# Kernel tuning notes

Hardware: AMD Instinct MI355X
Metric: run time of the kernel (lower is better)

The kernel has to match this reference:

```python
import jax, jax.numpy as jnp
import numpy as np

N_NEIGHBORS = 5


def setup_inputs() -> dict:
    key = jax.random.key(0)
    k1, k2, k3 = jax.random.split(key, 3)
    B, N, D = 2048, 100000, 128
    x = jax.random.normal(k1, (B, D), dtype=jnp.float32)
    train_data = jax.random.normal(k2, (N, D), dtype=jnp.float32)
    train_labels = jax.random.normal(k3, (N,), dtype=jnp.float32)
    return {"x": x, "train_data": train_data, "train_labels": train_labels}


def reference(x, train_data, train_labels):
    # Euclidean (minkowski p=2) pairwise distances [B, N] via the GEMM
    x2 = jnp.sum(x * x, axis=1, keepdims=True)            # [B,1]
    t2 = jnp.sum(train_data * train_data, axis=1)          # [N]
    d2 = x2 - 2.0 * (x @ train_data.T) + t2[None, :]       # [B,N]
    dist = jnp.sqrt(jnp.maximum(d2, 0.0))

    # k smallest distances (torch.topk largest=False)
    neg_d, idx = jax.lax.top_k(-dist, N_NEIGHBORS)         # [B,k]
    d = -neg_d

    labels = train_labels[idx]                             # [B,k]

    # weights = 'distance': inverse distance, with exact-match handling
    d_inv = 1.0 / d
    inf_mask = jnp.isinf(d_inv)
    inf_row = jnp.any(inf_mask, axis=1, keepdims=True)
    w = jnp.where(inf_row, inf_mask.astype(jnp.float32), d_inv)  # [B,k]

    out = jnp.sum(w * labels, axis=1) / jnp.sum(w, axis=1)  # [B]
    return out
```

## Files before the change

### kernel.cpp

```cpp
#include <hip/hip_runtime.h>
#include <math.h>

typedef __attribute__((ext_vector_type(8))) short bf16x8;
typedef __attribute__((ext_vector_type(4))) float f32x4;
typedef unsigned short ushortT;
typedef unsigned int uint32;

#define KNN_K   5
#define DIM     128
#define FLT_BIG 3.402823466e38f
#define KEY_C   512.0f

#define MF_B     2048
#define MF_N     100000
#define MF_QPB   256
#define MF_QPW   64
#define MF_NCH   250
#define MF_CHS   400
#define MF_TILES (MF_CHS / 16)
#define MF_CSLOT 4
#define MF_NCAND (MF_NCH * MF_CSLOT)
#define MF_RESCORE 10

__device__ __forceinline__ uint32 umn(uint32 a, uint32 b) { return a < b ? a : b; }
__device__ __forceinline__ uint32 umx(uint32 a, uint32 b) { return a > b ? a : b; }

#define TOP5_INSERT(v, id)                                                  \
    if ((v) < bd4) {                                                        \
        bool l0 = (v) < bd0, l1 = (v) < bd1, l2 = (v) < bd2, l3 = (v) < bd3;\
        if (l3) { bd4 = bd3; bi4 = bi3; } else { bd4 = (v); bi4 = (id); }   \
        if (l2) { bd3 = bd2; bi3 = bi2; } else if (l3) { bd3 = (v); bi3 = (id); } \
        if (l1) { bd2 = bd1; bi2 = bi1; } else if (l2) { bd2 = (v); bi2 = (id); } \
        if (l0) { bd1 = bd0; bi1 = bi0; } else if (l1) { bd1 = (v); bi1 = (id); } \
        if (l0) { bd0 = (v); bi0 = (id); }                                  \
    }

__device__ __forceinline__ uint32 f2bf_u(float f) {
    unsigned u = __float_as_uint(f);
    u += 0x7fffu + ((u >> 16) & 1u);
    return u >> 16;
}

__global__ __launch_bounds__(256) void prep_kernel(const float* __restrict__ in,
                                                   ushortT* __restrict__ outbf,
                                                   float* __restrict__ t2c, int rows) {
    const int wv = threadIdx.x >> 6, lane = threadIdx.x & 63;
    const int row = (blockIdx.x * 4 + wv) * 16 + (lane >> 2);
    if (row >= rows) return;
    const int seg = (lane & 3) * 32;
    const float4* p = (const float4*)(in + (size_t)row * DIM + seg);

    float4 v[8];
#pragma unroll
    for (int j = 0; j < 8; ++j) v[j] = p[j];

    uint32 u[16];
#pragma unroll
    for (int j = 0; j < 8; ++j) {
        u[2 * j]     = f2bf_u(v[j].x) | (f2bf_u(v[j].y) << 16);
        u[2 * j + 1] = f2bf_u(v[j].z) | (f2bf_u(v[j].w) << 16);
    }
    uint4* o = (uint4*)(outbf + (size_t)row * DIM + seg);
#pragma unroll
    for (int j = 0; j < 4; ++j)
        o[j] = make_uint4(u[4 * j], u[4 * j + 1], u[4 * j + 2], u[4 * j + 3]);

    float s = 0.f;
#pragma unroll
    for (int j = 0; j < 8; ++j)
        s += v[j].x * v[j].x + v[j].y * v[j].y + v[j].z * v[j].z + v[j].w * v[j].w;
    s += __shfl_xor(s, 1);
    s += __shfl_xor(s, 2);
    if ((lane & 3) == 0) t2c[row] = -(s + KEY_C) * 0.5f;
}

__global__ __launch_bounds__(256) void knn_mfma(
        const ushortT* __restrict__ xbf, const ushortT* __restrict__ tbf,
        const float* __restrict__ t2c,
        uint32* __restrict__ cand_k, uint32* __restrict__ cand_i) {
    __shared__ uint32 sk[4][MF_QPW][12];

    const int tid  = threadIdx.x;
    const int wv   = tid >> 6;
    const int lane = tid & 63;
    const int quad = lane >> 4;
    const int c16  = lane & 15;
    const int chunk = blockIdx.x;
    const int qbase = blockIdx.y * MF_QPB + wv * MF_QPW;
    const int n0 = chunk * MF_CHS;

    bf16x8 bq[4][4];
#pragma unroll
    for (int t = 0; t < 4; ++t)
#pragma unroll
        for (int s = 0; s < 4; ++s)
            bq[t][s] = *(const bf16x8*)(xbf + (size_t)(qbase + t * 16 + c16) * DIM
                                        + s * 32 + quad * 8);

    uint32 L[4][3];
#pragma unroll
    for (int t = 0; t < 4; ++t) { L[t][0] = 0xFFFFFFFFu; L[t][1] = 0xFFFFFFFFu; L[t][2] = 0xFFFFFFFFu; }

    const ushortT* ap = tbf + (size_t)(n0 + c16) * DIM + quad * 8;
    const float*   tp = t2c + n0 + quad * 4;

    bf16x8 fa[4];
#pragma unroll
    for (int s = 0; s < 4; ++s) fa[s] = *(const bf16x8*)(ap + s * 32);
    float4 tv = *(const float4*)tp;

    int locb = quad * 4;
    for (int tile = 0; tile < MF_TILES; ++tile) {
        const int nx = (tile + 1 < MF_TILES) ? tile + 1 : 0;
        const ushortT* np = ap + (size_t)nx * (16 * DIM);
        bf16x8 fb[4];
#pragma unroll
        for (int s = 0; s < 4; ++s) fb[s] = *(const bf16x8*)(np + s * 32);
        float4 tn = *(const float4*)(tp + nx * 16);

        f32x4 acc[4];
#pragma unroll
        for (int t = 0; t < 4; ++t) acc[t] = (f32x4){tv.x, tv.y, tv.z, tv.w};
#pragma unroll
        for (int s = 0; s < 4; ++s)
#pragma unroll
            for (int t = 0; t < 4; ++t)
                acc[t] = __builtin_amdgcn_mfma_f32_16x16x32_bf16(
                             fa[s], bq[t][s], acc[t], 0, 0, 0);

#pragma unroll
        for (int t = 0; t < 4; ++t) {
            uint32 p0 = (__float_as_uint(acc[t][0]) & 0xFFFFFC00u) | (uint32)(locb + 0);
            uint32 p1 = (__float_as_uint(acc[t][1]) & 0xFFFFFC00u) | (uint32)(locb + 1);
            uint32 p2 = (__float_as_uint(acc[t][2]) & 0xFFFFFC00u) | (uint32)(locb + 2);
            uint32 p3 = (__float_as_uint(acc[t][3]) & 0xFFFFFC00u) | (uint32)(locb + 3);
            uint32 m0 = umn(p0, p1), M0 = umx(p0, p1);
            uint32 m1 = umn(p2, p3), M1 = umx(p2, p3);
            uint32 s0 = umn(m0, m1);
            uint32 c  = umx(m0, m1), d = umn(M0, M1);
            uint32 s1 = umn(c, d),   s2 = umx(c, d);
            uint32 a0 = L[t][0], a1 = L[t][1], a2 = L[t][2];
            uint32 cc = umx(a0, s0), dd = umn(a1, s1);
            uint32 ee = umx(a1, s1), ff = umn(a2, s2);
            L[t][0] = umn(a0, s0);
            L[t][1] = umn(cc, dd);
            L[t][2] = umn(umx(cc, dd), umn(ee, ff));
        }
        locb += 16;
#pragma unroll
        for (int s = 0; s < 4; ++s) fa[s] = fb[s];
        tv = tn;
    }

#pragma unroll
    for (int t = 0; t < 4; ++t)
#pragma unroll
        for (int j = 0; j < 3; ++j)
            sk[wv][t * 16 + c16][quad * 3 + j] = L[t][j];
    __syncthreads();

    const int mw = tid >> 6, ml = tid & 63;
    uint32 k0 = 0xFFFFFFFFu, k1 = 0xFFFFFFFFu, k2 = 0xFFFFFFFFu, k3 = 0xFFFFFFFFu;
#pragma unroll
    for (int j = 0; j < 12; ++j) {
        uint32 v = sk[mw][ml][j];
        uint32 t0 = umx(k0, v);
        k0 = umn(k0, v);
        uint32 t1 = umx(k1, t0);
        k1 = umn(k1, t0);
        uint32 t2_ = umx(k2, t1);
        k2 = umn(k2, t1);
        k3 = umn(k3, t2_);
    }
    const size_t base = ((size_t)(blockIdx.y * MF_QPB + tid) * MF_NCH + chunk)
                        * MF_CSLOT;
    uint4 kk; kk.x = k0; kk.y = k1; kk.z = k2; kk.w = k3;
    uint4 ii; ii.x = n0 + (k0 & 1023u); ii.y = n0 + (k1 & 1023u);
    ii.z = n0 + (k2 & 1023u); ii.w = n0 + (k3 & 1023u);
    *(uint4*)(cand_k + base) = kk;
    *(uint4*)(cand_i + base) = ii;
}

__global__ __launch_bounds__(64) void knn_final(
        const uint32* __restrict__ cand_k, const uint32* __restrict__ cand_i,
        const float* __restrict__ x, const float* __restrict__ train,
        const float* __restrict__ labels, float* __restrict__ out) {
    const int q = blockIdx.x;
    const int lane = threadIdx.x;
    const float xa = x[(size_t)q * DIM + lane];
    const float xb = x[(size_t)q * DIM + 64 + lane];

    uint32 ck[16]; uint32 cid[16];
    const size_t cb = (size_t)q * MF_NCAND;
#pragma unroll
    for (int j = 0; j < 16; ++j) {
        int p = lane + 64 * j;
        if (p < MF_NCAND) { ck[j] = cand_k[cb + p]; cid[j] = cand_i[cb + p]; }
        else { ck[j] = 0xFFFFFFFFu; cid[j] = 0x7FFFFFFFu; }
    }

    uint32 selid[MF_RESCORE];
    uint32 tk = 0, ti = 0; bool first = true;
#pragma unroll
    for (int round = 0; round < MF_RESCORE; ++round) {
        uint32 mk = 0xFFFFFFFFu, mi = 0xFFFFFFFFu;
#pragma unroll
        for (int j = 0; j < 16; ++j) {
            bool gt = first || (ck[j] > tk) || (ck[j] == tk && cid[j] > ti);
            if (gt && ((ck[j] < mk) || (ck[j] == mk && cid[j] < mi))) {
                mk = ck[j]; mi = cid[j];
            }
        }
#pragma unroll
        for (int off = 32; off; off >>= 1) {
            uint32 ok = __shfl_xor(mk, off);
            uint32 oi = __shfl_xor(mi, off);
            if (ok < mk || (ok == mk && oi < mi)) { mk = ok; mi = oi; }
        }
        selid[round] = mi;
        tk = mk; ti = mi; first = false;
    }

    float d2v[MF_RESCORE];
#pragma unroll
    for (int r = 0; r < MF_RESCORE; ++r) {
        const float* tr = train + (size_t)selid[r] * DIM;
        float da = xa - tr[lane];
        float db = xb - tr[64 + lane];
        d2v[r] = fmaf(da, da, db * db);
    }
#pragma unroll
    for (int r = 0; r < MF_RESCORE; ++r) {
#pragma unroll
        for (int off = 32; off; off >>= 1) d2v[r] += __shfl_xor(d2v[r], off);
    }

    float bd0 = FLT_BIG, bd1 = FLT_BIG, bd2 = FLT_BIG, bd3 = FLT_BIG, bd4 = FLT_BIG;
    int   bi0 = 0, bi1 = 0, bi2 = 0, bi3 = 0, bi4 = 0;
#pragma unroll
    for (int r = 0; r < MF_RESCORE; ++r) {
        float v = d2v[r]; int id = (int)selid[r];
        TOP5_INSERT(v, id);
    }

    float d0 = sqrtf(fmaxf(bd0, 0.f));
    float d1 = sqrtf(fmaxf(bd1, 0.f));
    float d2_ = sqrtf(fmaxf(bd2, 0.f));
    float d3 = sqrtf(fmaxf(bd3, 0.f));
    float d4 = sqrtf(fmaxf(bd4, 0.f));
    bool zero = (d0 == 0.f) || (d1 == 0.f) || (d2_ == 0.f) || (d3 == 0.f) || (d4 == 0.f);
    float w0, w1, w2, w3, w4;
    if (zero) {
        w0 = (d0 == 0.f) ? 1.f : 0.f;
        w1 = (d1 == 0.f) ? 1.f : 0.f;
        w2 = (d2_ == 0.f) ? 1.f : 0.f;
        w3 = (d3 == 0.f) ? 1.f : 0.f;
        w4 = (d4 == 0.f) ? 1.f : 0.f;
    } else {
        w0 = 1.f / d0; w1 = 1.f / d1; w2 = 1.f / d2_; w3 = 1.f / d3; w4 = 1.f / d4;
    }
    float wsum = w0 + w1 + w2 + w3 + w4;
    float lsum = w0 * labels[bi0] + w1 * labels[bi1] + w2 * labels[bi2]
               + w3 * labels[bi3] + w4 * labels[bi4];
    if (lane == 0) out[q] = lsum / wsum;
}

#define FB_QT     16
#define FB_NCHUNK 25
#define FB_NT     256

__global__ void rowsq_kernel(const float* __restrict__ data,
                             float* __restrict__ out, int rows) {
    int r = blockIdx.x * blockDim.x + threadIdx.x;
    if (r >= rows) return;
    const float4* p = (const float4*)(data + (size_t)r * DIM);
    float s0 = 0.f, s1 = 0.f, s2 = 0.f, s3 = 0.f;
#pragma unroll
    for (int i = 0; i < DIM / 4; ++i) {
        float4 v = p[i];
        s0 += v.x * v.x; s1 += v.y * v.y; s2 += v.z * v.z; s3 += v.w * v.w;
    }
    out[r] = (s0 + s1) + (s2 + s3);
}

__global__ __launch_bounds__(FB_NT) void fb_phaseA(
        const float* __restrict__ x, const float* __restrict__ train,
        const float* __restrict__ x2, const float* __restrict__ t2,
        float* __restrict__ cand_d, int* __restrict__ cand_i,
        int N, int chunkSize) {
    __shared__ float xs[FB_QT][DIM + 4];
    __shared__ float rd[FB_QT][16 * KNN_K];
    __shared__ int   ri[FB_QT][16 * KNN_K];

    const int q0 = blockIdx.x * FB_QT;
    const int chunk = blockIdx.y;
    const int n0 = chunk * chunkSize;
    const int n1 = min(n0 + chunkSize, N);
    const int t = threadIdx.x;

    for (int i = t; i < FB_QT * DIM; i += FB_NT) {
        int q = i >> 7, d = i & (DIM - 1);
        xs[q][d] = x[(size_t)(q0 + q) * DIM + d];
    }
    __syncthreads();

    const int q  = t & (FB_QT - 1);
    const int ln = t >> 4;
    const float myx2 = x2[q0 + q];
    const float4* xp = (const float4*)xs[q];

    float bd0 = FLT_BIG, bd1 = FLT_BIG, bd2 = FLT_BIG, bd3 = FLT_BIG, bd4 = FLT_BIG;
    int   bi0 = -1, bi1 = -1, bi2 = -1, bi3 = -1, bi4 = -1;

    int n = n0 + ln;
    for (; n < n1; n += 16) {
        const float4* r0 = (const float4*)(train + (size_t)n * DIM);
        float dA = 0.f;
#pragma unroll 8
        for (int i = 0; i < DIM / 4; ++i) {
            float4 a = xp[i], b0 = r0[i];
            dA += a.x * b0.x + a.y * b0.y + a.z * b0.z + a.w * b0.w;
        }
        float vA = myx2 - 2.f * dA + t2[n];
        TOP5_INSERT(vA, n);
    }

    rd[q][ln * KNN_K + 0] = bd0;  ri[q][ln * KNN_K + 0] = bi0;
    rd[q][ln * KNN_K + 1] = bd1;  ri[q][ln * KNN_K + 1] = bi1;
    rd[q][ln * KNN_K + 2] = bd2;  ri[q][ln * KNN_K + 2] = bi2;
    rd[q][ln * KNN_K + 3] = bd3;  ri[q][ln * KNN_K + 3] = bi3;
    rd[q][ln * KNN_K + 4] = bd4;  ri[q][ln * KNN_K + 4] = bi4;
    __syncthreads();

    if (t < FB_QT) {
        float* dq = rd[t]; int* iq = ri[t];
        size_t base = ((size_t)(q0 + t) * FB_NCHUNK + chunk) * KNN_K;
#pragma unroll
        for (int k = 0; k < KNN_K; ++k) {
            float best = FLT_BIG; int bj = 0;
            for (int j = 0; j < 16 * KNN_K; ++j) {
                float v = dq[j];
                if (v < best) { best = v; bj = j; }
            }
            cand_d[base + k] = best; cand_i[base + k] = iq[bj];
            dq[bj] = FLT_BIG;
        }
    }
}

__global__ void fb_phaseB(const float* __restrict__ cand_d,
                          const int* __restrict__ cand_i,
                          const float* __restrict__ labels,
                          float* __restrict__ out, int B, int ncand) {
    int qq = blockIdx.x * blockDim.x + threadIdx.x;
    if (qq >= B) return;
    const float* cd = cand_d + (size_t)qq * ncand;
    const int*   ci = cand_i + (size_t)qq * ncand;

    float bd0 = FLT_BIG, bd1 = FLT_BIG, bd2 = FLT_BIG, bd3 = FLT_BIG, bd4 = FLT_BIG;
    int   bi0 = -1, bi1 = -1, bi2 = -1, bi3 = -1, bi4 = -1;
    for (int j = 0; j < ncand; ++j) {
        float v = cd[j]; int id = ci[j];
        TOP5_INSERT(v, id);
    }
    float d0 = sqrtf(fmaxf(bd0, 0.f));
    float d1 = sqrtf(fmaxf(bd1, 0.f));
    float d2 = sqrtf(fmaxf(bd2, 0.f));
    float d3 = sqrtf(fmaxf(bd3, 0.f));
    float d4 = sqrtf(fmaxf(bd4, 0.f));
    bool zero = (d0 == 0.f) || (d1 == 0.f) || (d2 == 0.f) || (d3 == 0.f) || (d4 == 0.f);
    float w0, w1, w2, w3, w4;
    if (zero) {
        w0 = (d0 == 0.f) ? 1.f : 0.f;
        w1 = (d1 == 0.f) ? 1.f : 0.f;
        w2 = (d2 == 0.f) ? 1.f : 0.f;
        w3 = (d3 == 0.f) ? 1.f : 0.f;
        w4 = (d4 == 0.f) ? 1.f : 0.f;
    } else {
        w0 = 1.f / d0; w1 = 1.f / d1; w2 = 1.f / d2; w3 = 1.f / d3; w4 = 1.f / d4;
    }
    float wsum = w0 + w1 + w2 + w3 + w4;
    float lsum = w0 * labels[bi0] + w1 * labels[bi1] + w2 * labels[bi2]
               + w3 * labels[bi3] + w4 * labels[bi4];
    out[qq] = lsum / wsum;
}

static inline size_t align256(size_t v) { return (v + 255) & ~(size_t)255; }

extern "C" void kernel_launch(void* const* d_in, const int* in_sizes, int n_in,
                              void* d_out, int out_size, void* d_ws, size_t ws_size,
                              hipStream_t stream) {
    const float* x      = (const float*)d_in[0];
    const float* train  = (const float*)d_in[1];
    const float* labels = (const float*)d_in[2];

    const int N = in_sizes[2];
    const int D = in_sizes[1] / N;
    const int B = in_sizes[0] / D;
    (void)n_in;

    size_t o_tbf = 0;
    size_t o_xbf = align256(o_tbf + (size_t)N * DIM * sizeof(ushortT));
    size_t o_t2c = align256(o_xbf + (size_t)B * DIM * sizeof(ushortT));
    size_t o_x2d = align256(o_t2c + (size_t)N * sizeof(float));
    size_t o_ck  = align256(o_x2d + (size_t)B * sizeof(float));
    size_t o_ci  = align256(o_ck + (size_t)B * MF_NCAND * sizeof(uint32));
    size_t need  = align256(o_ci + (size_t)B * MF_NCAND * sizeof(uint32));

    const bool mfma_ok = (N == MF_N) && (D == DIM) && (B == MF_B) && (ws_size >= need);

    if (mfma_ok) {
        ushortT* tbf = (ushortT*)((char*)d_ws + o_tbf);
        ushortT* xbf = (ushortT*)((char*)d_ws + o_xbf);
        float* t2c   = (float*)((char*)d_ws + o_t2c);
        float* x2d   = (float*)((char*)d_ws + o_x2d);
        uint32* cand_k = (uint32*)((char*)d_ws + o_ck);
        uint32* cand_i = (uint32*)((char*)d_ws + o_ci);

        prep_kernel<<<(N + 63) / 64, 256, 0, stream>>>(train, tbf, t2c, N);
        prep_kernel<<<(B + 63) / 64, 256, 0, stream>>>(x, xbf, x2d, B);

        dim3 gridA(MF_NCH, MF_B / MF_QPB);
        knn_mfma<<<gridA, 256, 0, stream>>>(xbf, tbf, t2c, cand_k, cand_i);
        knn_final<<<MF_B, 64, 0, stream>>>(cand_k, cand_i, x, train, labels,
                                           (float*)d_out);
    } else {
        float* t2     = (float*)d_ws;
        float* x2v    = t2 + N;
        float* cand_d = x2v + B;
        int*   cand_i = (int*)(cand_d + (size_t)B * FB_NCHUNK * KNN_K);

        rowsq_kernel<<<(N + 255) / 256, 256, 0, stream>>>(train, t2, N);
        rowsq_kernel<<<(B + 255) / 256, 256, 0, stream>>>(x, x2v, B);
        const int chunkSize = (N + FB_NCHUNK - 1) / FB_NCHUNK;
        dim3 gridA(B / FB_QT, FB_NCHUNK);
        fb_phaseA<<<gridA, FB_NT, 0, stream>>>(x, train, x2v, t2,
                                               cand_d, cand_i, N, chunkSize);
        fb_phaseB<<<(B + 255) / 256, 256, 0, stream>>>(cand_d, cand_i, labels,
                                                       (float*)d_out, B,
                                                       FB_NCHUNK * KNN_K);
    }
}
```

Baseline: 237.1 us.

## Pad train chunks to 256, swizzle block mapping, drop candidate index buffer

Pads the training set to 256 chunks, with padding rows given a sentinel norm term, so the candidate count per query divides evenly into the final-kernel lanes. The 2D grid becomes a 1D launch whose block ids are swizzled so groups of 8 chunks are processed across all 8 query groups together, aiming for better L2 reuse of train tiles. Candidate indices are no longer written to memory; the final kernel rebuilds them from slot position and the low key bits, halving candidate traffic. The tile loop is manually double-buffered in pairs. The cost is a few extra padded chunks of work, and the padding keys must never be selected.

```diff
diff --git a/kernel.cpp b/kernel.cpp
--- a/kernel.cpp
+++ b/kernel.cpp
@@ -15,9 +15,10 @@
 #define MF_N     100000
 #define MF_QPB   256
 #define MF_QPW   64
-#define MF_NCH   250
+#define MF_NCH   256
 #define MF_CHS   400
-#define MF_TILES (MF_CHS / 16)
+#define MF_NPAD  (MF_NCH * MF_CHS)
+#define MF_TILES 25
 #define MF_CSLOT 4
 #define MF_NCAND (MF_NCH * MF_CSLOT)
 #define MF_RESCORE 10
@@ -43,10 +44,15 @@
 
 __global__ __launch_bounds__(256) void prep_kernel(const float* __restrict__ in,
                                                    ushortT* __restrict__ outbf,
-                                                   float* __restrict__ t2c, int rows) {
+                                                   float* __restrict__ t2c,
+                                                   int rowsValid, int rowsTotal) {
     const int wv = threadIdx.x >> 6, lane = threadIdx.x & 63;
     const int row = (blockIdx.x * 4 + wv) * 16 + (lane >> 2);
-    if (row >= rows) return;
+    if (row >= rowsTotal) return;
+    if (row >= rowsValid) {
+        if ((lane & 3) == 0) t2c[row] = -1e30f;
+        return;
+    }
     const int seg = (lane & 3) * 32;
     const float4* p = (const float4*)(in + (size_t)row * DIM + seg);
 
@@ -76,17 +82,19 @@
 
 __global__ __launch_bounds__(256) void knn_mfma(
         const ushortT* __restrict__ xbf, const ushortT* __restrict__ tbf,
-        const float* __restrict__ t2c,
-        uint32* __restrict__ cand_k, uint32* __restrict__ cand_i) {
+        const float* __restrict__ t2c, uint32* __restrict__ cand_k) {
     __shared__ uint32 sk[4][MF_QPW][12];
 
+    const int id   = blockIdx.x;
+    const int r8   = id & 7, g = id >> 3;
+    const int chunk = ((g >> 3) << 3) | r8;
+    const int jq   = g & 7;
     const int tid  = threadIdx.x;
     const int wv   = tid >> 6;
     const int lane = tid & 63;
     const int quad = lane >> 4;
     const int c16  = lane & 15;
-    const int chunk = blockIdx.x;
-    const int qbase = blockIdx.y * MF_QPB + wv * MF_QPW;
+    const int qbase = jq * MF_QPB + wv * MF_QPW;
     const int n0 = chunk * MF_CHS;
 
     bf16x8 bq[4][4];
@@ -104,20 +112,7 @@
     const ushortT* ap = tbf + (size_t)(n0 + c16) * DIM + quad * 8;
     const float*   tp = t2c + n0 + quad * 4;
 
-    bf16x8 fa[4];
-#pragma unroll
-    for (int s = 0; s < 4; ++s) fa[s] = *(const bf16x8*)(ap + s * 32);
-    float4 tv = *(const float4*)tp;
-
-    int locb = quad * 4;
-    for (int tile = 0; tile < MF_TILES; ++tile) {
-        const int nx = (tile + 1 < MF_TILES) ? tile + 1 : 0;
-        const ushortT* np = ap + (size_t)nx * (16 * DIM);
-        bf16x8 fb[4];
-#pragma unroll
-        for (int s = 0; s < 4; ++s) fb[s] = *(const bf16x8*)(np + s * 32);
-        float4 tn = *(const float4*)(tp + nx * 16);
-
+    auto process = [&](bf16x8 (&F)[4], float4 tv, int locb) {
         f32x4 acc[4];
 #pragma unroll
         for (int t = 0; t < 4; ++t) acc[t] = (f32x4){tv.x, tv.y, tv.z, tv.w};
@@ -126,8 +121,7 @@
 #pragma unroll
             for (int t = 0; t < 4; ++t)
                 acc[t] = __builtin_amdgcn_mfma_f32_16x16x32_bf16(
-                             fa[s], bq[t][s], acc[t], 0, 0, 0);
-
+                             F[s], bq[t][s], acc[t], 0, 0, 0);
 #pragma unroll
         for (int t = 0; t < 4; ++t) {
             uint32 p0 = (__float_as_uint(acc[t][0]) & 0xFFFFFC00u) | (uint32)(locb + 0);
@@ -146,11 +140,27 @@
             L[t][1] = umn(cc, dd);
             L[t][2] = umn(umx(cc, dd), umn(ee, ff));
         }
-        locb += 16;
-#pragma unroll
-        for (int s = 0; s < 4; ++s) fa[s] = fb[s];
-        tv = tn;
-    }
+    };
+
+    bf16x8 fa[4], fb[4];
+    float4 tva, tvb;
+#pragma unroll
+    for (int s = 0; s < 4; ++s) fa[s] = *(const bf16x8*)(ap + s * 32);
+    tva = *(const float4*)tp;
+
+    int locb = quad * 4;
+    for (int it = 0; it < 12; ++it) {
+#pragma unroll
+        for (int s = 0; s < 4; ++s) fb[s] = *(const bf16x8*)(ap + 16 * DIM + s * 32);
+        tvb = *(const float4*)(tp + 16);
+        process(fa, tva, locb);
+#pragma unroll
+        for (int s = 0; s < 4; ++s) fa[s] = *(const bf16x8*)(ap + 32 * DIM + s * 32);
+        tva = *(const float4*)(tp + 32);
+        process(fb, tvb, locb + 16);
+        ap += 32 * DIM; tp += 32; locb += 32;
+    }
+    process(fa, tva, locb);
 
 #pragma unroll
     for (int t = 0; t < 4; ++t)
@@ -172,17 +182,13 @@
         k2 = umn(k2, t1);
         k3 = umn(k3, t2_);
     }
-    const size_t base = ((size_t)(blockIdx.y * MF_QPB + tid) * MF_NCH + chunk)
-                        * MF_CSLOT;
+    const size_t base = ((size_t)(jq * MF_QPB + tid) * MF_NCH + chunk) * MF_CSLOT;
     uint4 kk; kk.x = k0; kk.y = k1; kk.z = k2; kk.w = k3;
-    uint4 ii; ii.x = n0 + (k0 & 1023u); ii.y = n0 + (k1 & 1023u);
-    ii.z = n0 + (k2 & 1023u); ii.w = n0 + (k3 & 1023u);
     *(uint4*)(cand_k + base) = kk;
-    *(uint4*)(cand_i + base) = ii;
 }
 
 __global__ __launch_bounds__(64) void knn_final(
-        const uint32* __restrict__ cand_k, const uint32* __restrict__ cand_i,
+        const uint32* __restrict__ cand_k,
         const float* __restrict__ x, const float* __restrict__ train,
         const float* __restrict__ labels, float* __restrict__ out) {
     const int q = blockIdx.x;
@@ -194,9 +200,10 @@
     const size_t cb = (size_t)q * MF_NCAND;
 #pragma unroll
     for (int j = 0; j < 16; ++j) {
-        int p = lane + 64 * j;
-        if (p < MF_NCAND) { ck[j] = cand_k[cb + p]; cid[j] = cand_i[cb + p]; }
-        else { ck[j] = 0xFFFFFFFFu; cid[j] = 0x7FFFFFFFu; }
+        const int p = lane + 64 * j;
+        uint32 k = cand_k[cb + p];
+        ck[j] = k;
+        cid[j] = (uint32)(p >> 2) * MF_CHS + (k & 1023u);
     }
 
     uint32 selid[MF_RESCORE];
@@ -400,12 +407,10 @@
     (void)n_in;
 
     size_t o_tbf = 0;
-    size_t o_xbf = align256(o_tbf + (size_t)N * DIM * sizeof(ushortT));
+    size_t o_xbf = align256(o_tbf + (size_t)MF_NPAD * DIM * sizeof(ushortT));
     size_t o_t2c = align256(o_xbf + (size_t)B * DIM * sizeof(ushortT));
-    size_t o_x2d = align256(o_t2c + (size_t)N * sizeof(float));
-    size_t o_ck  = align256(o_x2d + (size_t)B * sizeof(float));
-    size_t o_ci  = align256(o_ck + (size_t)B * MF_NCAND * sizeof(uint32));
-    size_t need  = align256(o_ci + (size_t)B * MF_NCAND * sizeof(uint32));
+    size_t o_ck  = align256(o_t2c + (size_t)MF_NPAD * sizeof(float));
+    size_t need  = align256(o_ck + (size_t)B * MF_NCAND * sizeof(uint32));
 
     const bool mfma_ok = (N == MF_N) && (D == DIM) && (B == MF_B) && (ws_size >= need);
 
@@ -413,16 +418,13 @@
         ushortT* tbf = (ushortT*)((char*)d_ws + o_tbf);
         ushortT* xbf = (ushortT*)((char*)d_ws + o_xbf);
         float* t2c   = (float*)((char*)d_ws + o_t2c);
-        float* x2d   = (float*)((char*)d_ws + o_x2d);
         uint32* cand_k = (uint32*)((char*)d_ws + o_ck);
-        uint32* cand_i = (uint32*)((char*)d_ws + o_ci);
-
-        prep_kernel<<<(N + 63) / 64, 256, 0, stream>>>(train, tbf, t2c, N);
-        prep_kernel<<<(B + 63) / 64, 256, 0, stream>>>(x, xbf, x2d, B);
-
-        dim3 gridA(MF_NCH, MF_B / MF_QPB);
-        knn_mfma<<<gridA, 256, 0, stream>>>(xbf, tbf, t2c, cand_k, cand_i);
-        knn_final<<<MF_B, 64, 0, stream>>>(cand_k, cand_i, x, train, labels,
+
+        prep_kernel<<<MF_NPAD / 64, 256, 0, stream>>>(train, tbf, t2c, N, MF_NPAD);
+        prep_kernel<<<(B + 63) / 64, 256, 0, stream>>>(x, xbf, (float*)cand_k, B, B);
+
+        knn_mfma<<<MF_NCH * 8, 256, 0, stream>>>(xbf, tbf, t2c, cand_k);
+        knn_final<<<MF_B, 64, 0, stream>>>(cand_k, x, train, labels,
                                            (float*)d_out);
     } else {
         float* t2     = (float*)d_ws;
```

Measured after the change: 238.9 us. No clear change (+0.8%).
